# Kernel tuning notes

Hardware: AMD Instinct MI355X
Metric: run time of the kernel (lower is better)

The kernel has to match this reference:

```python
import jax, jax.numpy as jnp
import numpy as np

DT = 0.1
LN_EPS = 1e-5
B, T, D_IN, H, N_APP = 128, 2048, 16, 256, 10


def layer_norm(x, g, b):
    mu = jnp.mean(x, axis=-1, keepdims=True)
    var = jnp.mean(jnp.square(x - mu), axis=-1, keepdims=True)
    return (x - mu) * jax.lax.rsqrt(var + LN_EPS) * g + b


def setup_inputs() -> dict:
    key = jax.random.key(0)
    ks = jax.random.split(key, 4)
    x = jax.random.normal(ks[0], (B, T, D_IN), dtype=jnp.float32)
    W_in = jax.random.normal(ks[1], (H, D_IN), dtype=jnp.float32) * (1.0 / np.sqrt(D_IN))
    b_in = jnp.zeros((H,), dtype=jnp.float32)
    tau_param = jnp.ones((H,), dtype=jnp.float32)
    # xavier_uniform for (H, H)
    limit = np.sqrt(6.0 / (H + H))
    W_rec = jax.random.uniform(ks[2], (H, H), dtype=jnp.float32, minval=-limit, maxval=limit)
    g_intra = jnp.ones((H,), dtype=jnp.float32)
    b_intra = jnp.zeros((H,), dtype=jnp.float32)
    g_norm = jnp.ones((H,), dtype=jnp.float32)
    b_norm = jnp.zeros((H,), dtype=jnp.float32)
    W_head = jax.random.normal(ks[3], (H, N_APP), dtype=jnp.float32) * (1.0 / np.sqrt(H))
    b_head = jnp.zeros((N_APP,), dtype=jnp.float32)
    return dict(x=x, W_in=W_in, b_in=b_in, tau_param=tau_param, W_rec=W_rec,
                g_intra=g_intra, b_intra=b_intra, g_norm=g_norm, b_norm=b_norm,
                W_head=W_head, b_head=b_head)


def reference(x, W_in, b_in, tau_param, W_rec, g_intra, b_intra, g_norm, b_norm, W_head, b_head):
    # x: (B, T, D_IN)
    tau = jax.nn.softplus(tau_param)  # (H,), fixed
    # Precompute input projection for all timesteps: (B, T, H)
    inp_proj = jnp.einsum('bti,hi->bth', x, W_in) + b_in
    xs = jnp.swapaxes(inp_proj, 0, 1)  # (T, B, H) for scan

    def step(h, u_t):
        rec = h @ W_rec                       # (B, H)
        f_t = jnp.tanh(layer_norm(u_t + rec, g_intra, b_intra))
        dh = (-h / tau + f_t) * DT
        h_new = jnp.clip(h + dh, -10.0, 10.0)
        return h_new, None

    h0 = jnp.zeros((x.shape[0], W_rec.shape[0]), dtype=x.dtype)
    h, _ = jax.lax.scan(step, h0, xs)
    h = layer_norm(h, g_norm, b_norm)
    return h @ W_head + b_head  # (B, N_APP)
```

## Files before the change

### kernel.cpp

```cpp
#include <hip/hip_runtime.h>


#define BB     128
#define TT     2048
#define DIN    16
#define HH     256
#define NAPP   10
#define DT_STEP 0.1f
#define LN_EPS_C 1e-5f

typedef _Float16 half2_t __attribute__((ext_vector_type(2)));

template<int CTRL>
__device__ __forceinline__ float dpp_mov0(float x) {
    return __builtin_bit_cast(float,
        __builtin_amdgcn_update_dpp(0, __builtin_bit_cast(int, x), CTRL, 0xF, 0xF, true));
}

__device__ __forceinline__ void wave_reduce2(float& s1, float& s2) {
    s1 += dpp_mov0<0x111>(s1); s2 += dpp_mov0<0x111>(s2);
    s1 += dpp_mov0<0x112>(s1); s2 += dpp_mov0<0x112>(s2);
    s1 += dpp_mov0<0x114>(s1); s2 += dpp_mov0<0x114>(s2);
    s1 += dpp_mov0<0x118>(s1); s2 += dpp_mov0<0x118>(s2);
    s1 += dpp_mov0<0x142>(s1); s2 += dpp_mov0<0x142>(s2);
    s1 += dpp_mov0<0x143>(s1); s2 += dpp_mov0<0x143>(s2);
}

__device__ __forceinline__ half2_t as_h2(int v) { return __builtin_bit_cast(half2_t, v); }

__global__ __launch_bounds__(256, 1)
void liquid_scan_kernel(const float* __restrict__ x,
                        const float* __restrict__ W_in,
                        const float* __restrict__ b_in,
                        const float* __restrict__ tau_param,
                        const float* __restrict__ W_rec,
                        const float* __restrict__ g_intra,
                        const float* __restrict__ b_intra,
                        const float* __restrict__ g_norm,
                        const float* __restrict__ b_norm,
                        const float* __restrict__ W_head,
                        const float* __restrict__ b_head,
                        float* __restrict__ out)
{
    const int tid  = threadIdx.x;
    const int b    = blockIdx.x;
    const int j    = tid;
    const int wv   = tid >> 6;
    const int lane = tid & 63;

    __shared__ __align__(16) float h_lds[HH];
    __shared__ __align__(16) float wred[4][2];
    __shared__ __align__(16) float xbuf[2][DIN];
    __shared__ float part[HH];

    half2_t w2[128];
    #pragma unroll
    for (int p = 0; p < 128; ++p) {
        const float wa = W_rec[(size_t)(2 * p)     * HH + j];
        const float wb = W_rec[(size_t)(2 * p + 1) * HH + j];
        half2_t t2; t2.x = (_Float16)wa; t2.y = (_Float16)wb;
        w2[p] = t2;
    }

    float win[DIN];
    #pragma unroll
    for (int k = 0; k < DIN; ++k)
        win[k] = W_in[j * DIN + k];

    const float bi   = b_in[j];
    const float gi   = g_intra[j];
    const float bbi  = b_intra[j];
    const float gn   = g_norm[j];
    const float bn   = b_norm[j];
    const float tp   = tau_param[j];
    const float tau  = (tp > 20.f) ? tp : log1pf(__expf(tp));
    const float itau = 1.f / tau;

    float hj   = 0.f;
    int   hpk0 = 0;
    int   hpk1 = 0;

    const size_t xbase = (size_t)b * TT * DIN;
    if (tid < DIN) xbuf[0][tid] = x[xbase + tid];
    __syncthreads();

    const int pl = tid - (256 - DIN);

    for (int t = 0; t < TT; ++t) {
        float xv = 0.f;
        if (pl >= 0 && t + 1 < TT)
            xv = x[xbase + (size_t)(t + 1) * DIN + pl];

        float a0 = 0.f, a1 = 0.f, a2 = 0.f, a3 = 0.f;
        #pragma unroll
        for (int p = 0; p < 64; p += 4) {
            const int s0 = __builtin_amdgcn_readlane(hpk0, p + 0);
            const int s1i = __builtin_amdgcn_readlane(hpk0, p + 1);
            const int s2i = __builtin_amdgcn_readlane(hpk0, p + 2);
            const int s3i = __builtin_amdgcn_readlane(hpk0, p + 3);
            a0 = __builtin_amdgcn_fdot2(as_h2(s0),  w2[p + 0], a0, false);
            a1 = __builtin_amdgcn_fdot2(as_h2(s1i), w2[p + 1], a1, false);
            a2 = __builtin_amdgcn_fdot2(as_h2(s2i), w2[p + 2], a2, false);
            a3 = __builtin_amdgcn_fdot2(as_h2(s3i), w2[p + 3], a3, false);
        }
        #pragma unroll
        for (int p = 0; p < 64; p += 4) {
            const int s0 = __builtin_amdgcn_readlane(hpk1, p + 0);
            const int s1i = __builtin_amdgcn_readlane(hpk1, p + 1);
            const int s2i = __builtin_amdgcn_readlane(hpk1, p + 2);
            const int s3i = __builtin_amdgcn_readlane(hpk1, p + 3);
            a0 = __builtin_amdgcn_fdot2(as_h2(s0),  w2[64 + p + 0], a0, false);
            a1 = __builtin_amdgcn_fdot2(as_h2(s1i), w2[64 + p + 1], a1, false);
            a2 = __builtin_amdgcn_fdot2(as_h2(s2i), w2[64 + p + 2], a2, false);
            a3 = __builtin_amdgcn_fdot2(as_h2(s3i), w2[64 + p + 3], a3, false);
        }
        const float acc = (a0 + a1) + (a2 + a3);

        float uin = bi;
        {
            const float4* xb = (const float4*)xbuf[t & 1];
            const float4 x0 = xb[0], x1 = xb[1], x2 = xb[2], x3 = xb[3];
            uin = fmaf(x0.x, win[0],  uin); uin = fmaf(x0.y, win[1],  uin);
            uin = fmaf(x0.z, win[2],  uin); uin = fmaf(x0.w, win[3],  uin);
            uin = fmaf(x1.x, win[4],  uin); uin = fmaf(x1.y, win[5],  uin);
            uin = fmaf(x1.z, win[6],  uin); uin = fmaf(x1.w, win[7],  uin);
            uin = fmaf(x2.x, win[8],  uin); uin = fmaf(x2.y, win[9],  uin);
            uin = fmaf(x2.z, win[10], uin); uin = fmaf(x2.w, win[11], uin);
            uin = fmaf(x3.x, win[12], uin); uin = fmaf(x3.y, win[13], uin);
            uin = fmaf(x3.z, win[14], uin); uin = fmaf(x3.w, win[15], uin);
        }

        const float u = uin + acc;

        float s1 = u, s2 = u * u;
        wave_reduce2(s1, s2);
        if (lane == 63) { wred[wv][0] = s1; wred[wv][1] = s2; }
        __syncthreads();

        const float4 ra = ((const float4*)wred)[0];
        const float4 rb = ((const float4*)wred)[1];
        const float S1 = (ra.x + ra.z) + (rb.x + rb.z);
        const float S2 = (ra.y + ra.w) + (rb.y + rb.w);
        const float mu  = S1 * (1.f / HH);
        const float var = S2 * (1.f / HH) - mu * mu;
        const float rs  = rsqrtf(var + LN_EPS_C);
        const float xn  = (u - mu) * rs * gi + bbi;
        const float e = __expf(2.f * xn);
        const float f = 1.f - 2.f / (e + 1.f);
        float hn = hj + (f - hj * itau) * DT_STEP;
        hn = fminf(10.f, fmaxf(-10.f, hn));
        hj = hn;
        h_lds[j] = hn;
        if (pl >= 0 && t + 1 < TT)
            xbuf[(t + 1) & 1][pl] = xv;
        __syncthreads();

        {
            const float2* hp2 = (const float2*)h_lds;
            const float2 h0 = hp2[lane];
            const float2 h1 = hp2[lane + 64];
            hpk0 = __builtin_bit_cast(int, __builtin_amdgcn_cvt_pkrtz(h0.x, h0.y));
            hpk1 = __builtin_bit_cast(int, __builtin_amdgcn_cvt_pkrtz(h1.x, h1.y));
        }
    }

    {
        float s1 = hj, s2 = hj * hj;
        wave_reduce2(s1, s2);
        if (lane == 63) { wred[wv][0] = s1; wred[wv][1] = s2; }
    }
    __syncthreads();
    {
        const float4 ra = ((const float4*)wred)[0];
        const float4 rb = ((const float4*)wred)[1];
        const float S1 = (ra.x + ra.z) + (rb.x + rb.z);
        const float S2 = (ra.y + ra.w) + (rb.y + rb.w);
        const float mu  = S1 * (1.f / HH);
        const float var = S2 * (1.f / HH) - mu * mu;
        const float rs  = rsqrtf(var + LN_EPS_C);
        part[j] = (hj - mu) * rs * gn + bn;
    }
    __syncthreads();
    if (tid < NAPP) {
        float o = b_head[tid];
        for (int jj = 0; jj < HH; ++jj)
            o = fmaf(part[jj], W_head[jj * NAPP + tid], o);
        out[(size_t)b * NAPP + tid] = o;
    }
}

extern "C" void kernel_launch(void* const* d_in, const int* in_sizes, int n_in,
                              void* d_out, int out_size, void* d_ws, size_t ws_size,
                              hipStream_t stream) {
    const float* x       = (const float*)d_in[0];
    const float* W_in    = (const float*)d_in[1];
    const float* b_in    = (const float*)d_in[2];
    const float* tau     = (const float*)d_in[3];
    const float* W_rec   = (const float*)d_in[4];
    const float* g_intra = (const float*)d_in[5];
    const float* b_intra = (const float*)d_in[6];
    const float* g_norm  = (const float*)d_in[7];
    const float* b_norm  = (const float*)d_in[8];
    const float* W_head  = (const float*)d_in[9];
    const float* b_head  = (const float*)d_in[10];
    float* out = (float*)d_out;

    hipLaunchKernelGGL(liquid_scan_kernel, dim3(BB), dim3(256), 0, stream,
                       x, W_in, b_in, tau, W_rec, g_intra, b_intra,
                       g_norm, b_norm, W_head, b_head, out);
}
```

Before: 1.872 ms.

## Split recurrent matvec across four thread slices with LDS partial-sum reduction

Launches 1024 threads per batch row instead of 256, with each group of 256 threads computing a quarter of the W_rec dot product over 64 hidden inputs. Partial sums go through shared memory and are combined by the first slice, which then runs layer norm, tanh and the state update. The packed fp16 hidden state is written directly to LDS by even lanes. This shortens the per-wave serial dot chain and raises the number of waves per CU, at the cost of an extra block barrier per timestep and more LDS traffic.

```diff
diff --git a/kernel.cpp b/kernel.cpp
--- a/kernel.cpp
+++ b/kernel.cpp
@@ -6,6 +6,7 @@
 #define DIN    16
 #define HH     256
 #define NAPP   10
+#define NT     1024
 #define DT_STEP 0.1f
 #define LN_EPS_C 1e-5f
 
@@ -28,7 +29,7 @@
 
 __device__ __forceinline__ half2_t as_h2(int v) { return __builtin_bit_cast(half2_t, v); }
 
-__global__ __launch_bounds__(256, 1)
+__global__ __launch_bounds__(NT, 1)
 void liquid_scan_kernel(const float* __restrict__ x,
                         const float* __restrict__ W_in,
                         const float* __restrict__ b_in,
@@ -44,80 +45,71 @@
 {
     const int tid  = threadIdx.x;
     const int b    = blockIdx.x;
-    const int j    = tid;
+    const int j    = tid & (HH - 1);
+    const int s    = tid >> 8;
     const int wv   = tid >> 6;
     const int lane = tid & 63;
 
-    __shared__ __align__(16) float h_lds[HH];
+    __shared__ float part[4][HH];
     __shared__ __align__(16) float wred[4][2];
     __shared__ __align__(16) float xbuf[2][DIN];
-    __shared__ float part[HH];
-
-    half2_t w2[128];
+    __shared__ unsigned int hpk_lds[HH / 2];
+
+    half2_t w2[32];
     #pragma unroll
-    for (int p = 0; p < 128; ++p) {
-        const float wa = W_rec[(size_t)(2 * p)     * HH + j];
-        const float wb = W_rec[(size_t)(2 * p + 1) * HH + j];
+    for (int p = 0; p < 32; ++p) {
+        const float wa = W_rec[(size_t)(s * 64 + 2 * p)     * HH + j];
+        const float wb = W_rec[(size_t)(s * 64 + 2 * p + 1) * HH + j];
         half2_t t2; t2.x = (_Float16)wa; t2.y = (_Float16)wb;
         w2[p] = t2;
     }
 
     float win[DIN];
-    #pragma unroll
-    for (int k = 0; k < DIN; ++k)
-        win[k] = W_in[j * DIN + k];
-
-    const float bi   = b_in[j];
-    const float gi   = g_intra[j];
-    const float bbi  = b_intra[j];
-    const float gn   = g_norm[j];
-    const float bn   = b_norm[j];
-    const float tp   = tau_param[j];
-    const float tau  = (tp > 20.f) ? tp : log1pf(__expf(tp));
-    const float itau = 1.f / tau;
-
-    float hj   = 0.f;
-    int   hpk0 = 0;
-    int   hpk1 = 0;
-
+    float bi = 0.f;
+    if (s == 1) {
+        bi = b_in[j];
+        #pragma unroll
+        for (int k = 0; k < DIN; ++k) win[k] = W_in[j * DIN + k];
+    }
+    float gi = 0.f, bbi = 0.f, gn = 0.f, bn = 0.f, itau = 0.f;
+    if (s == 0) {
+        gi = g_intra[j]; bbi = b_intra[j]; gn = g_norm[j]; bn = b_norm[j];
+        const float tp  = tau_param[j];
+        const float tau = (tp > 20.f) ? tp : log1pf(__expf(tp));
+        itau = 1.f / tau;
+    }
+
+    float hj = 0.f;
+    if (tid < HH / 2) hpk_lds[tid] = 0u;
     const size_t xbase = (size_t)b * TT * DIN;
     if (tid < DIN) xbuf[0][tid] = x[xbase + tid];
     __syncthreads();
 
-    const int pl = tid - (256 - DIN);
+    const int pl = tid - (NT - DIN);
 
     for (int t = 0; t < TT; ++t) {
         float xv = 0.f;
         if (pl >= 0 && t + 1 < TT)
             xv = x[xbase + (size_t)(t + 1) * DIN + pl];
 
+        const int hpk = (int)hpk_lds[(s << 5) + (lane & 31)];
+
         float a0 = 0.f, a1 = 0.f, a2 = 0.f, a3 = 0.f;
         #pragma unroll
-        for (int p = 0; p < 64; p += 4) {
-            const int s0 = __builtin_amdgcn_readlane(hpk0, p + 0);
-            const int s1i = __builtin_amdgcn_readlane(hpk0, p + 1);
-            const int s2i = __builtin_amdgcn_readlane(hpk0, p + 2);
-            const int s3i = __builtin_amdgcn_readlane(hpk0, p + 3);
-            a0 = __builtin_amdgcn_fdot2(as_h2(s0),  w2[p + 0], a0, false);
-            a1 = __builtin_amdgcn_fdot2(as_h2(s1i), w2[p + 1], a1, false);
-            a2 = __builtin_amdgcn_fdot2(as_h2(s2i), w2[p + 2], a2, false);
-            a3 = __builtin_amdgcn_fdot2(as_h2(s3i), w2[p + 3], a3, false);
-        }
-        #pragma unroll
-        for (int p = 0; p < 64; p += 4) {
-            const int s0 = __builtin_amdgcn_readlane(hpk1, p + 0);
-            const int s1i = __builtin_amdgcn_readlane(hpk1, p + 1);
-            const int s2i = __builtin_amdgcn_readlane(hpk1, p + 2);
-            const int s3i = __builtin_amdgcn_readlane(hpk1, p + 3);
-            a0 = __builtin_amdgcn_fdot2(as_h2(s0),  w2[64 + p + 0], a0, false);
-            a1 = __builtin_amdgcn_fdot2(as_h2(s1i), w2[64 + p + 1], a1, false);
-            a2 = __builtin_amdgcn_fdot2(as_h2(s2i), w2[64 + p + 2], a2, false);
-            a3 = __builtin_amdgcn_fdot2(as_h2(s3i), w2[64 + p + 3], a3, false);
-        }
-        const float acc = (a0 + a1) + (a2 + a3);
-
-        float uin = bi;
-        {
+        for (int p = 0; p < 32; p += 4) {
+            const int r0 = __builtin_amdgcn_readlane(hpk, p + 0);
+            const int r1 = __builtin_amdgcn_readlane(hpk, p + 1);
+            const int r2 = __builtin_amdgcn_readlane(hpk, p + 2);
+            const int r3 = __builtin_amdgcn_readlane(hpk, p + 3);
+            a0 = __builtin_amdgcn_fdot2(as_h2(r0), w2[p + 0], a0, false);
+            a1 = __builtin_amdgcn_fdot2(as_h2(r1), w2[p + 1], a1, false);
+            a2 = __builtin_amdgcn_fdot2(as_h2(r2), w2[p + 2], a2, false);
+            a3 = __builtin_amdgcn_fdot2(as_h2(r3), w2[p + 3], a3, false);
+        }
+        float acc = (a0 + a1) + (a2 + a3);
+
+        if (s == 1) {
+            float uin = bi;
             const float4* xb = (const float4*)xbuf[t & 1];
             const float4 x0 = xb[0], x1 = xb[1], x2 = xb[2], x3 = xb[3];
             uin = fmaf(x0.x, win[0],  uin); uin = fmaf(x0.y, win[1],  uin);
@@ -128,15 +120,54 @@
             uin = fmaf(x2.z, win[10], uin); uin = fmaf(x2.w, win[11], uin);
             uin = fmaf(x3.x, win[12], uin); uin = fmaf(x3.y, win[13], uin);
             uin = fmaf(x3.z, win[14], uin); uin = fmaf(x3.w, win[15], uin);
-        }
-
-        const float u = uin + acc;
-
-        float s1 = u, s2 = u * u;
+            part[1][j] = acc + uin;
+        } else if (s >= 2) {
+            part[s][j] = acc;
+        }
+        __syncthreads();
+
+        float u_carry = 0.f;
+        if (tid < HH) {
+            const float u = acc + (part[1][j] + part[2][j]) + part[3][j];
+            u_carry = u;
+            float s1 = u, s2 = u * u;
+            wave_reduce2(s1, s2);
+            if (lane == 63) { wred[wv][0] = s1; wred[wv][1] = s2; }
+        }
+        __syncthreads();
+
+        if (tid < HH) {
+            const float4 ra = ((const float4*)wred)[0];
+            const float4 rb = ((const float4*)wred)[1];
+            const float S1 = (ra.x + ra.z) + (rb.x + rb.z);
+            const float S2 = (ra.y + ra.w) + (rb.y + rb.w);
+            const float mu  = S1 * (1.f / HH);
+            const float var = S2 * (1.f / HH) - mu * mu;
+            const float rs  = rsqrtf(var + LN_EPS_C);
+            const float xn  = (u_carry - mu) * rs * gi + bbi;
+            const float e = __expf(2.f * xn);
+            const float f = 1.f - 2.f / (e + 1.f);
+            float hn = hj + (f - hj * itau) * DT_STEP;
+            hn = fminf(10.f, fmaxf(-10.f, hn));
+            hj = hn;
+            const float hnb = __builtin_bit_cast(float,
+                __builtin_amdgcn_update_dpp(0, __builtin_bit_cast(int, hn), 0x101, 0xF, 0xF, true));
+            if (!(lane & 1))
+                hpk_lds[j >> 1] = __builtin_bit_cast(unsigned int,
+                                   __builtin_amdgcn_cvt_pkrtz(hn, hnb));
+        } else if (pl >= 0 && t + 1 < TT) {
+            xbuf[(t + 1) & 1][pl] = xv;
+        }
+        __syncthreads();
+    }
+
+    if (tid < HH) {
+        float s1 = hj, s2 = hj * hj;
         wave_reduce2(s1, s2);
         if (lane == 63) { wred[wv][0] = s1; wred[wv][1] = s2; }
-        __syncthreads();
-
+    }
+    __syncthreads();
+    if (tid < HH) {
         const float4 ra = ((const float4*)wred)[0];
         const float4 rb = ((const float4*)wred)[1];
         const float S1 = (ra.x + ra.z) + (rb.x + rb.z);
@@ -144,47 +175,13 @@
         const float mu  = S1 * (1.f / HH);
         const float var = S2 * (1.f / HH) - mu * mu;
         const float rs  = rsqrtf(var + LN_EPS_C);
-        const float xn  = (u - mu) * rs * gi + bbi;
-        const float e = __expf(2.f * xn);
-        const float f = 1.f - 2.f / (e + 1.f);
-        float hn = hj + (f - hj * itau) * DT_STEP;
-        hn = fminf(10.f, fmaxf(-10.f, hn));
-        hj = hn;
-        h_lds[j] = hn;
-        if (pl >= 0 && t + 1 < TT)
-            xbuf[(t + 1) & 1][pl] = xv;
-        __syncthreads();
-
-        {
-            const float2* hp2 = (const float2*)h_lds;
-            const float2 h0 = hp2[lane];
-            const float2 h1 = hp2[lane + 64];
-            hpk0 = __builtin_bit_cast(int, __builtin_amdgcn_cvt_pkrtz(h0.x, h0.y));
-            hpk1 = __builtin_bit_cast(int, __builtin_amdgcn_cvt_pkrtz(h1.x, h1.y));
-        }
-    }
-
-    {
-        float s1 = hj, s2 = hj * hj;
-        wave_reduce2(s1, s2);
-        if (lane == 63) { wred[wv][0] = s1; wred[wv][1] = s2; }
-    }
-    __syncthreads();
-    {
-        const float4 ra = ((const float4*)wred)[0];
-        const float4 rb = ((const float4*)wred)[1];
-        const float S1 = (ra.x + ra.z) + (rb.x + rb.z);
-        const float S2 = (ra.y + ra.w) + (rb.y + rb.w);
-        const float mu  = S1 * (1.f / HH);
-        const float var = S2 * (1.f / HH) - mu * mu;
-        const float rs  = rsqrtf(var + LN_EPS_C);
-        part[j] = (hj - mu) * rs * gn + bn;
+        part[0][j] = (hj - mu) * rs * gn + bn;
     }
     __syncthreads();
     if (tid < NAPP) {
         float o = b_head[tid];
         for (int jj = 0; jj < HH; ++jj)
-            o = fmaf(part[jj], W_head[jj * NAPP + tid], o);
+            o = fmaf(part[0][jj], W_head[jj * NAPP + tid], o);
         out[(size_t)b * NAPP + tid] = o;
     }
 }
@@ -205,7 +202,7 @@
     const float* b_head  = (const float*)d_in[10];
     float* out = (float*)d_out;
 
-    hipLaunchKernelGGL(liquid_scan_kernel, dim3(BB), dim3(256), 0, stream,
+    hipLaunchKernelGGL(liquid_scan_kernel, dim3(BB), dim3(NT), 0, stream,
                        x, W_in, b_in, tau, W_rec, g_intra, b_intra,
                        g_norm, b_norm, W_head, b_head, out);
 }
```

After: 1.962 ms. 4.8% more time.
